# Performance work log

Measured on AMD Instinct MI355X. Metric: run time of the kernel, lower is better.

## Reference

```python
import jax, jax.numpy as jnp
import numpy as np

A_DIM = 12      # action dim (half of augmented state)
N_STEPS = 10    # Heun ODE steps (Flow.N)
P = 0.95        # mixing coefficient in _Heun_method


def _mlp(x, obs, t, W1, b1, W2, b2, W3, b3, W4, b4):
    h = jnp.concatenate([x, obs, t], axis=-1)
    h = jnp.tanh(h @ W1 + b1)
    h = jnp.tanh(h @ W2 + b2)
    h = jnp.tanh(h @ W3 + b3)
    return h @ W4 + b4


def _heun(obs, x, params):
    # Flow._Heun_method: sequential Heun integration of the augmented state.
    z = x[..., :A_DIM]
    y = x[..., A_DIM:]
    dt = 1.0 / N_STEPS
    tshape = x.shape[:-1] + (1,)

    def step(carry, i):
        z, y = carry
        t = jnp.ones(tshape, x.dtype) * (i / N_STEPS)
        z_t = _mlp(y, obs, t, *params)
        z_in = z + z_t * dt
        y_t = _mlp(z_in, obs, t, *params)
        y_in = y + y_t * dt
        z_new = P * z_in + (1.0 - P) * y_in
        y_new = P * y_in + (1.0 - P) * z_new
        return (z_new, y_new), None

    (z, y), _ = jax.lax.scan(step, (z, y), jnp.arange(N_STEPS, dtype=x.dtype))
    return jnp.concatenate([z, y], axis=-1)


def setup_inputs() -> dict:
    key = jax.random.key(0)
    ks = jax.random.split(key, 8)
    B, OBS, H, A = 2048, 48, 256, A_DIM
    din = A + OBS + 1  # 61
    s = 0.05  # small init scale to keep tanh unsaturated
    return {
        "observations": jax.random.normal(ks[0], (B, OBS), jnp.float32),
        "action_aug_0": jax.random.normal(ks[1], (B, 2 * A), jnp.float32),
        "W1": s * jax.random.normal(ks[2], (din, H), jnp.float32),
        "b1": jnp.zeros((H,), jnp.float32),
        "W2": s * jax.random.normal(ks[3], (H, H), jnp.float32),
        "b2": jnp.zeros((H,), jnp.float32),
        "W3": s * jax.random.normal(ks[4], (H, H), jnp.float32),
        "b3": jnp.zeros((H,), jnp.float32),
        "W4": s * jax.random.normal(ks[5], (H, A), jnp.float32),
        "b4": jnp.zeros((A,), jnp.float32),
        "jac": 1,
    }


def reference(observations, action_aug_0, W1, b1, W2, b2, W3, b3, W4, b4, jac):
    params = (W1, b1, W2, b2, W3, b3, W4, b4)
    action_aug = _heun(observations, action_aug_0, params)
    d = action_aug_0.shape[-1]
    # Normal(0, I) log prob summed over dims
    log_probs = -0.5 * jnp.sum(action_aug_0 ** 2, axis=-1) - 0.5 * d * jnp.log(2.0 * jnp.pi)
    if jac:
        single = lambda o, x: _heun(o, x, params)  # per-sample (obs_dim,), (2a,)
        J = jax.vmap(jax.jacrev(single, argnums=1))(observations, action_aug_0)  # (B, 2a, 2a)
        _, logabsdet = jnp.linalg.slogdet(J)  # = log|det J|
        log_probs = log_probs - logabsdet
    return action_aug, log_probs
```

## Files before the change

kernel.cpp:

```cpp
#include <hip/hip_runtime.h>
#include <hip/hip_bf16.h>


typedef unsigned short ushort_t;
typedef float f32x4 __attribute__((ext_vector_type(4)));
typedef short s16x8 __attribute__((ext_vector_type(8)));

#define NB      2048
#define OBS_D   48
#define HDIM    256
#define ADIM    12
#define XDIM    24
#define NSTEPS  10
#define DT      0.1f
#define PP      0.95f

#define W1U 0
#define W2U 16384
#define W3U 81920
#define W4U 147456
#define N_FRAG 151552
#define FRAG_BLOCKS 592
#define LP_BLOCKS 8

#define LDS_BUFA 0
#define LDS_BUFB 9216
#define LDS_AIN  18432
#define LDS_PART 21504
#define LDS_TOTAL 31744

__device__ __forceinline__ ushort_t f2bf(float f) {
  unsigned u = __builtin_bit_cast(unsigned, f);
  u += 0x7fffu + ((u >> 16) & 1u);
  return (ushort_t)(u >> 16);
}

__device__ __forceinline__ float tanh_fast(float x) {
  float e = __builtin_amdgcn_exp2f(x * 2.885390081777927f);
  return 1.f - 2.f * __builtin_amdgcn_rcpf(1.f + e);
}

__device__ __forceinline__ int ain_byte(int r, int c) {
  return r * 192 + ((c >> 5) << 6) + ((c & 15) << 2) + (((c >> 4) & 1) << 1);
}

__global__ void prep_kernel(const float* __restrict__ W1, const float* __restrict__ b1,
                            const float* __restrict__ W2, const float* __restrict__ W3,
                            const float* __restrict__ W4, const float* __restrict__ x0,
                            const int* __restrict__ jac, float* __restrict__ out,
                            ushort_t* __restrict__ ws) {
  int bid = blockIdx.x;
  int tid = threadIdx.x;
  if (bid < FRAG_BLOCKS) {
    int e = bid * 256 + tid;
    float val = 0.f;
    if (e < 16384) {
      int kt = e >> 13; int r = e & 8191;
      int nt = r >> 9, l = (r >> 3) & 63, j = r & 7;
      int k = kt * 32 + ((l >> 4) << 2) + (j >> 1) + ((j & 1) << 4);
      int col = nt * 16 + (l & 15);
      val = (k < 61) ? W1[k * 256 + col] : ((k == 61) ? b1[col] : 0.f);
    } else if (e < 81920) {
      int e2 = e - 16384;
      int kt = e2 >> 13; int r = e2 & 8191;
      int nt = r >> 9, l = (r >> 3) & 63, j = r & 7;
      int k = kt * 32 + ((l >> 4) << 2) + (j >> 1) + ((j & 1) << 4);
      int col = nt * 16 + (l & 15);
      val = W2[k * 256 + col];
    } else if (e < 147456) {
      int e2 = e - 81920;
      int kt = e2 >> 13; int r = e2 & 8191;
      int nt = r >> 9, l = (r >> 3) & 63, j = r & 7;
      int k = kt * 32 + ((l >> 4) << 2) + (j >> 1) + ((j & 1) << 4);
      int col = nt * 16 + (l & 15);
      val = W3[k * 256 + col];
    } else {
      int e2 = e - 147456;
      int kt = e2 >> 9; int r = e2 & 511;
      int l = (r >> 3) & 63, j = r & 7;
      int k = kt * 32 + ((l >> 4) << 2) + (j >> 1) + ((j & 1) << 4);
      int col = l & 15;
      val = (col < 12) ? W4[k * 12 + col] : 0.f;
    }
    ws[e] = f2bf(val);
  } else {
    int s = (bid - FRAG_BLOCKS) * 256 + tid;
    float acc = 0.f;
    #pragma unroll 4
    for (int j = 0; j < XDIM; ++j) { float v = x0[s * XDIM + j]; acc += v * v; }
    float C = (jac[0] != 0) ? -9.744134143900015f : -22.054524796912143f;
    out[NB * XDIM + s] = -0.5f * acc + C;
  }
}

__global__ __launch_bounds__(512, 2) void flow_main(
    const float* __restrict__ obs, const float* __restrict__ x0,
    const float* __restrict__ b2g, const float* __restrict__ b3g,
    const float* __restrict__ b4g, const ushort_t* __restrict__ ws,
    float* __restrict__ out) {
  __shared__ char lds[LDS_TOTAL];
  const int tid  = threadIdx.x;
  const int lane = tid & 63;
  const int wv   = tid >> 6;
  const int g    = lane >> 4;
  const int ar   = lane & 15;
  const int row0 = blockIdx.x * 16;

  const int aA = LDS_AIN + ar * 192 + g * 16;
  const int hA = ar * 576 + (((ar >> 2) & 1) << 6) + g * 16;
  const int hw = (g * 4) * 576 + ((g & 1) << 6) + wv * 64 + ar * 4;
  const int pw = LDS_PART + wv * 1280 + (g * 4) * 80 + ar * 4;
  const int rs = tid >> 4, cs = tid & 15;

  for (int p = tid; p < 768; p += 512) ((unsigned*)(lds + LDS_AIN))[p] = 0u;
  __syncthreads();

  for (int idx = tid; idx < 16 * OBS_D; idx += 512) {
    int r = idx / OBS_D, o = idx - r * OBS_D;
    *(ushort_t*)(lds + LDS_AIN + ain_byte(r, 12 + o)) = f2bf(obs[(row0 + r) * OBS_D + o]);
  }
  if (tid < 16)
    *(ushort_t*)(lds + LDS_AIN + tid * 192 + 118) = (ushort_t)0x3F80;

  float zr = 0.f, yr = 0.f, zir = 0.f;
  if (tid < 256 && cs < 12) {
    zr = x0[(row0 + rs) * XDIM + cs];
    yr = x0[(row0 + rs) * XDIM + 12 + cs];
    *(ushort_t*)(lds + LDS_AIN + rs * 192 + cs * 4) = f2bf(yr);
  }

  s16x8 w1r[2][2], w2r[8][2], w3r[8][2], w4r;
  #pragma unroll
  for (int kt = 0; kt < 2; ++kt)
    #pragma unroll
    for (int n = 0; n < 2; ++n)
      w1r[kt][n] = *(const s16x8*)(ws + W1U + (((kt * 16) + (2 * wv + n)) * 64 + lane) * 8);
  #pragma unroll
  for (int kt = 0; kt < 8; ++kt)
    #pragma unroll
    for (int n = 0; n < 2; ++n) {
      w2r[kt][n] = *(const s16x8*)(ws + W2U + (((kt * 16) + (2 * wv + n)) * 64 + lane) * 8);
      w3r[kt][n] = *(const s16x8*)(ws + W3U + (((kt * 16) + (2 * wv + n)) * 64 + lane) * 8);
    }
  w4r = *(const s16x8*)(ws + W4U + (wv * 64 + lane) * 8);

  float b2r[2], b3r[2];
  #pragma unroll
  for (int n = 0; n < 2; ++n) {
    b2r[n] = b2g[(2 * wv + n) * 16 + ar];
    b3r[n] = b3g[(2 * wv + n) * 16 + ar];
  }
  const float b4v = (cs < 12) ? b4g[cs] : 0.f;

  __syncthreads();

  const f32x4 z4 = {0.f, 0.f, 0.f, 0.f};

  for (int i = 0; i < NSTEPS; ++i) {
    #pragma unroll
    for (int ev = 0; ev < 2; ++ev) {
      f32x4 acc0 = z4, acc1 = z4;
      #pragma unroll
      for (int kt = 0; kt < 2; ++kt) {
        s16x8 a = *(const s16x8*)(lds + aA + kt * 64);
        acc0 = __builtin_amdgcn_mfma_f32_16x16x32_bf16(a, w1r[kt][0], acc0, 0, 0, 0);
        acc1 = __builtin_amdgcn_mfma_f32_16x16x32_bf16(a, w1r[kt][1], acc1, 0, 0, 0);
      }
      #pragma unroll
      for (int r = 0; r < 4; ++r) {
        unsigned p = (unsigned)f2bf(tanh_fast(acc0[r]))
                   | ((unsigned)f2bf(tanh_fast(acc1[r])) << 16);
        *(unsigned*)(lds + LDS_BUFA + hw + r * 576) = p;
      }
      __syncthreads();

      acc0 = z4; acc1 = z4;
      #pragma unroll
      for (int kt = 0; kt < 8; ++kt) {
        s16x8 a = *(const s16x8*)(lds + LDS_BUFA + hA + kt * 64);
        acc0 = __builtin_amdgcn_mfma_f32_16x16x32_bf16(a, w2r[kt][0], acc0, 0, 0, 0);
        acc1 = __builtin_amdgcn_mfma_f32_16x16x32_bf16(a, w2r[kt][1], acc1, 0, 0, 0);
      }
      #pragma unroll
      for (int r = 0; r < 4; ++r) {
        unsigned p = (unsigned)f2bf(tanh_fast(acc0[r] + b2r[0]))
                   | ((unsigned)f2bf(tanh_fast(acc1[r] + b2r[1])) << 16);
        *(unsigned*)(lds + LDS_BUFB + hw + r * 576) = p;
      }
      __syncthreads();

      acc0 = z4; acc1 = z4;
      #pragma unroll
      for (int kt = 0; kt < 8; ++kt) {
        s16x8 a = *(const s16x8*)(lds + LDS_BUFB + hA + kt * 64);
        acc0 = __builtin_amdgcn_mfma_f32_16x16x32_bf16(a, w3r[kt][0], acc0, 0, 0, 0);
        acc1 = __builtin_amdgcn_mfma_f32_16x16x32_bf16(a, w3r[kt][1], acc1, 0, 0, 0);
      }
      #pragma unroll
      for (int r = 0; r < 4; ++r) {
        unsigned p = (unsigned)f2bf(tanh_fast(acc0[r] + b3r[0]))
                   | ((unsigned)f2bf(tanh_fast(acc1[r] + b3r[1])) << 16);
        *(unsigned*)(lds + LDS_BUFA + hw + r * 576) = p;
      }

      asm volatile("s_waitcnt lgkmcnt(0)" ::: "memory");
      __builtin_amdgcn_sched_barrier(0);
      {
        s16x8 a = *(const s16x8*)(lds + LDS_BUFA + hA + wv * 64);
        f32x4 p4 = __builtin_amdgcn_mfma_f32_16x16x32_bf16(a, w4r, z4, 0, 0, 0);
        #pragma unroll
        for (int r = 0; r < 4; ++r)
          *(float*)(lds + pw + r * 80) = p4[r];
      }
      __syncthreads();

      if (tid < 256) {
        float s = b4v;
        #pragma unroll
        for (int w = 0; w < 8; ++w)
          s += *(const float*)(lds + LDS_PART + w * 1280 + rs * 80 + cs * 4);
        if (cs < 12) {
          if (ev == 0) {
            zir = zr + DT * s;
            *(ushort_t*)(lds + LDS_AIN + rs * 192 + cs * 4) = f2bf(zir);
          } else {
            float yi = yr + DT * s;
            zr = PP * zir + (1.f - PP) * yi;
            yr = PP * yi + (1.f - PP) * zr;
            *(ushort_t*)(lds + LDS_AIN + rs * 192 + cs * 4) = f2bf(yr);
          }
        }
        if (ev == 1 && cs == 15)
          *(ushort_t*)(lds + LDS_AIN + rs * 192 + 114) = f2bf((float)(i + 1) * DT);
      }
      __syncthreads();
    }
  }

  if (tid < 256 && cs < 12) {
    out[(row0 + rs) * XDIM + cs]      = zr;
    out[(row0 + rs) * XDIM + 12 + cs] = yr;
  }
}

extern "C" void kernel_launch(void* const* d_in, const int* in_sizes, int n_in,
                              void* d_out, int out_size, void* d_ws, size_t ws_size,
                              hipStream_t stream) {
  const float* obs = (const float*)d_in[0];
  const float* x0  = (const float*)d_in[1];
  const float* W1  = (const float*)d_in[2];
  const float* b1  = (const float*)d_in[3];
  const float* W2  = (const float*)d_in[4];
  const float* b2  = (const float*)d_in[5];
  const float* W3  = (const float*)d_in[6];
  const float* b3  = (const float*)d_in[7];
  const float* W4  = (const float*)d_in[8];
  const float* b4  = (const float*)d_in[9];
  const int*   jac = (const int*)d_in[10];
  float* out = (float*)d_out;
  ushort_t* ws = (ushort_t*)d_ws;

  prep_kernel<<<FRAG_BLOCKS + LP_BLOCKS, 256, 0, stream>>>(W1, b1, W2, W3, W4, x0, jac, out, ws);
  flow_main<<<128, 512, 0, stream>>>(obs, x0, b2, b3, b4, ws, out);
}
```

Measured before the change: 49.71 us.

## Halve rows per block, swizzle LDS layout, split MFMA accumulator chains

Each block now handles 8 real rows instead of 16 and the grid doubles to 256 blocks, so more CUs take part in the sequential Heun loop. The padded LDS layouts are replaced with XOR-swizzled 128/512-byte row layouts to avoid bank conflicts at lower memory cost. The 8-deep MFMA accumulation for layers 2 and 3 is split into two independent chains that are summed afterwards, shortening the dependency latency. Empty asm constraints pin the weight fragments in registers. The cost is that half of each MFMA tile now works on padding rows, and the full weight set is loaded by twice as many blocks.

Measured after the change: 50.84 us. 2.3% more time.

```diff
diff --git a/kernel.cpp b/kernel.cpp
--- a/kernel.cpp
+++ b/kernel.cpp
@@ -8,8 +8,6 @@
 
 #define NB      2048
 #define OBS_D   48
-#define HDIM    256
-#define ADIM    12
 #define XDIM    24
 #define NSTEPS  10
 #define DT      0.1f
@@ -19,15 +17,14 @@
 #define W2U 16384
 #define W3U 81920
 #define W4U 147456
-#define N_FRAG 151552
 #define FRAG_BLOCKS 592
 #define LP_BLOCKS 8
 
 #define LDS_BUFA 0
-#define LDS_BUFB 9216
-#define LDS_AIN  18432
-#define LDS_PART 21504
-#define LDS_TOTAL 31744
+#define LDS_BUFB 8192
+#define LDS_AIN  16384
+#define LDS_PART 18432
+#define LDS_TOTAL 27648
 
 __device__ __forceinline__ ushort_t f2bf(float f) {
   unsigned u = __builtin_bit_cast(unsigned, f);
@@ -41,7 +38,8 @@
 }
 
 __device__ __forceinline__ int ain_byte(int r, int c) {
-  return r * 192 + ((c >> 5) << 6) + ((c & 15) << 2) + (((c >> 4) & 1) << 1);
+  int cb = ((c >> 5) << 6) | ((c & 15) << 2) | (((c >> 4) & 1) << 1);
+  return r * 128 + (cb ^ ((r & 7) << 4));
 }
 
 __global__ void prep_kernel(const float* __restrict__ W1, const float* __restrict__ b1,
@@ -104,29 +102,26 @@
   const int wv   = tid >> 6;
   const int g    = lane >> 4;
   const int ar   = lane & 15;
-  const int row0 = blockIdx.x * 16;
-
-  const int aA = LDS_AIN + ar * 192 + g * 16;
-  const int hA = ar * 576 + (((ar >> 2) & 1) << 6) + g * 16;
-  const int hw = (g * 4) * 576 + ((g & 1) << 6) + wv * 64 + ar * 4;
-  const int pw = LDS_PART + wv * 1280 + (g * 4) * 80 + ar * 4;
-  const int rs = tid >> 4, cs = tid & 15;
-
-  for (int p = tid; p < 768; p += 512) ((unsigned*)(lds + LDS_AIN))[p] = 0u;
+  const int row0 = blockIdx.x * 8;
+  const int sw   = (ar & 7) << 4;
+  const int hwc  = wv * 64 + ar * 4;
+  const int rs   = tid >> 4, cs = tid & 15;
+
+  ((unsigned*)(lds + LDS_AIN))[tid] = 0u;
   __syncthreads();
 
-  for (int idx = tid; idx < 16 * OBS_D; idx += 512) {
-    int r = idx / OBS_D, o = idx - r * OBS_D;
+  if (tid < 8 * OBS_D) {
+    int r = tid / OBS_D, o = tid - r * OBS_D;
     *(ushort_t*)(lds + LDS_AIN + ain_byte(r, 12 + o)) = f2bf(obs[(row0 + r) * OBS_D + o]);
   }
   if (tid < 16)
-    *(ushort_t*)(lds + LDS_AIN + tid * 192 + 118) = (ushort_t)0x3F80;
+    *(ushort_t*)(lds + LDS_AIN + tid * 128 + (118 ^ ((tid & 7) << 4))) = (ushort_t)0x3F80;
 
   float zr = 0.f, yr = 0.f, zir = 0.f;
-  if (tid < 256 && cs < 12) {
+  if (tid < 256 && cs < 12 && rs < 8) {
     zr = x0[(row0 + rs) * XDIM + cs];
     yr = x0[(row0 + rs) * XDIM + 12 + cs];
-    *(ushort_t*)(lds + LDS_AIN + rs * 192 + cs * 4) = f2bf(yr);
+    *(ushort_t*)(lds + LDS_AIN + rs * 128 + ((cs * 4) ^ ((rs & 7) << 4))) = f2bf(yr);
   }
 
   s16x8 w1r[2][2], w2r[8][2], w3r[8][2], w4r;
@@ -143,6 +138,13 @@
       w3r[kt][n] = *(const s16x8*)(ws + W3U + (((kt * 16) + (2 * wv + n)) * 64 + lane) * 8);
     }
   w4r = *(const s16x8*)(ws + W4U + (wv * 64 + lane) * 8);
+  #pragma unroll
+  for (int kt = 0; kt < 2; ++kt)
+    asm volatile("" : "+v"(w1r[kt][0]), "+v"(w1r[kt][1]));
+  #pragma unroll
+  for (int kt = 0; kt < 8; ++kt)
+    asm volatile("" : "+v"(w2r[kt][0]), "+v"(w2r[kt][1]), "+v"(w3r[kt][0]), "+v"(w3r[kt][1]));
+  asm volatile("" : "+v"(w4r));
 
   float b2r[2], b3r[2];
   #pragma unroll
@@ -162,55 +164,68 @@
       f32x4 acc0 = z4, acc1 = z4;
       #pragma unroll
       for (int kt = 0; kt < 2; ++kt) {
-        s16x8 a = *(const s16x8*)(lds + aA + kt * 64);
+        s16x8 a = *(const s16x8*)(lds + LDS_AIN + ar * 128 + ((kt * 64 + g * 16) ^ sw));
         acc0 = __builtin_amdgcn_mfma_f32_16x16x32_bf16(a, w1r[kt][0], acc0, 0, 0, 0);
         acc1 = __builtin_amdgcn_mfma_f32_16x16x32_bf16(a, w1r[kt][1], acc1, 0, 0, 0);
       }
       #pragma unroll
       for (int r = 0; r < 4; ++r) {
+        int rw = g * 4 + r;
         unsigned p = (unsigned)f2bf(tanh_fast(acc0[r]))
                    | ((unsigned)f2bf(tanh_fast(acc1[r])) << 16);
-        *(unsigned*)(lds + LDS_BUFA + hw + r * 576) = p;
-      }
-      __syncthreads();
-
-      acc0 = z4; acc1 = z4;
-      #pragma unroll
-      for (int kt = 0; kt < 8; ++kt) {
-        s16x8 a = *(const s16x8*)(lds + LDS_BUFA + hA + kt * 64);
-        acc0 = __builtin_amdgcn_mfma_f32_16x16x32_bf16(a, w2r[kt][0], acc0, 0, 0, 0);
-        acc1 = __builtin_amdgcn_mfma_f32_16x16x32_bf16(a, w2r[kt][1], acc1, 0, 0, 0);
-      }
+        *(unsigned*)(lds + LDS_BUFA + rw * 512 + (hwc ^ ((rw & 7) << 4))) = p;
+      }
+      __syncthreads();
+
+      f32x4 a0a = z4, a0b = z4, a1a = z4, a1b = z4;
+      #pragma unroll
+      for (int kt = 0; kt < 4; ++kt) {
+        s16x8 a = *(const s16x8*)(lds + LDS_BUFA + ar * 512 + ((kt * 64 + g * 16) ^ sw));
+        s16x8 b = *(const s16x8*)(lds + LDS_BUFA + ar * 512 + (((kt + 4) * 64 + g * 16) ^ sw));
+        a0a = __builtin_amdgcn_mfma_f32_16x16x32_bf16(a, w2r[kt][0], a0a, 0, 0, 0);
+        a1a = __builtin_amdgcn_mfma_f32_16x16x32_bf16(a, w2r[kt][1], a1a, 0, 0, 0);
+        a0b = __builtin_amdgcn_mfma_f32_16x16x32_bf16(b, w2r[kt + 4][0], a0b, 0, 0, 0);
+        a1b = __builtin_amdgcn_mfma_f32_16x16x32_bf16(b, w2r[kt + 4][1], a1b, 0, 0, 0);
+      }
+      acc0 = a0a + a0b; acc1 = a1a + a1b;
       #pragma unroll
       for (int r = 0; r < 4; ++r) {
+        int rw = g * 4 + r;
         unsigned p = (unsigned)f2bf(tanh_fast(acc0[r] + b2r[0]))
                    | ((unsigned)f2bf(tanh_fast(acc1[r] + b2r[1])) << 16);
-        *(unsigned*)(lds + LDS_BUFB + hw + r * 576) = p;
-      }
-      __syncthreads();
-
-      acc0 = z4; acc1 = z4;
-      #pragma unroll
-      for (int kt = 0; kt < 8; ++kt) {
-        s16x8 a = *(const s16x8*)(lds + LDS_BUFB + hA + kt * 64);
-        acc0 = __builtin_amdgcn_mfma_f32_16x16x32_bf16(a, w3r[kt][0], acc0, 0, 0, 0);
-        acc1 = __builtin_amdgcn_mfma_f32_16x16x32_bf16(a, w3r[kt][1], acc1, 0, 0, 0);
-      }
+        *(unsigned*)(lds + LDS_BUFB + rw * 512 + (hwc ^ ((rw & 7) << 4))) = p;
+      }
+      __syncthreads();
+
+      a0a = z4; a0b = z4; a1a = z4; a1b = z4;
+      #pragma unroll
+      for (int kt = 0; kt < 4; ++kt) {
+        s16x8 a = *(const s16x8*)(lds + LDS_BUFB + ar * 512 + ((kt * 64 + g * 16) ^ sw));
+        s16x8 b = *(const s16x8*)(lds + LDS_BUFB + ar * 512 + (((kt + 4) * 64 + g * 16) ^ sw));
+        a0a = __builtin_amdgcn_mfma_f32_16x16x32_bf16(a, w3r[kt][0], a0a, 0, 0, 0);
+        a1a = __builtin_amdgcn_mfma_f32_16x16x32_bf16(a, w3r[kt][1], a1a, 0, 0, 0);
+        a0b = __builtin_amdgcn_mfma_f32_16x16x32_bf16(b, w3r[kt + 4][0], a0b, 0, 0, 0);
+        a1b = __builtin_amdgcn_mfma_f32_16x16x32_bf16(b, w3r[kt + 4][1], a1b, 0, 0, 0);
+      }
+      acc0 = a0a + a0b; acc1 = a1a + a1b;
       #pragma unroll
       for (int r = 0; r < 4; ++r) {
+        int rw = g * 4 + r;
         unsigned p = (unsigned)f2bf(tanh_fast(acc0[r] + b3r[0]))
                    | ((unsigned)f2bf(tanh_fast(acc1[r] + b3r[1])) << 16);
-        *(unsigned*)(lds + LDS_BUFA + hw + r * 576) = p;
+        *(unsigned*)(lds + LDS_BUFA + rw * 512 + (hwc ^ ((rw & 7) << 4))) = p;
       }
 
       asm volatile("s_waitcnt lgkmcnt(0)" ::: "memory");
       __builtin_amdgcn_sched_barrier(0);
       {
-        s16x8 a = *(const s16x8*)(lds + LDS_BUFA + hA + wv * 64);
+        s16x8 a = *(const s16x8*)(lds + LDS_BUFA + ar * 512 + ((wv * 64 + g * 16) ^ sw));
         f32x4 p4 = __builtin_amdgcn_mfma_f32_16x16x32_bf16(a, w4r, z4, 0, 0, 0);
         #pragma unroll
-        for (int r = 0; r < 4; ++r)
-          *(float*)(lds + pw + r * 80) = p4[r];
+        for (int r = 0; r < 4; ++r) {
+          int rw = g * 4 + r;
+          *(float*)(lds + LDS_PART + wv * 1152 + rw * 72 + ar * 4) = p4[r];
+        }
       }
       __syncthreads();
 
@@ -218,26 +233,28 @@
         float s = b4v;
         #pragma unroll
         for (int w = 0; w < 8; ++w)
-          s += *(const float*)(lds + LDS_PART + w * 1280 + rs * 80 + cs * 4);
+          s += *(const float*)(lds + LDS_PART + w * 1152 + rs * 72 + cs * 4);
         if (cs < 12) {
+          int byt = rs * 128 + ((cs * 4) ^ ((rs & 7) << 4));
           if (ev == 0) {
             zir = zr + DT * s;
-            *(ushort_t*)(lds + LDS_AIN + rs * 192 + cs * 4) = f2bf(zir);
+            *(ushort_t*)(lds + LDS_AIN + byt) = f2bf(zir);
           } else {
             float yi = yr + DT * s;
             zr = PP * zir + (1.f - PP) * yi;
             yr = PP * yi + (1.f - PP) * zr;
-            *(ushort_t*)(lds + LDS_AIN + rs * 192 + cs * 4) = f2bf(yr);
+            *(ushort_t*)(lds + LDS_AIN + byt) = f2bf(yr);
           }
         }
         if (ev == 1 && cs == 15)
-          *(ushort_t*)(lds + LDS_AIN + rs * 192 + 114) = f2bf((float)(i + 1) * DT);
+          *(ushort_t*)(lds + LDS_AIN + rs * 128 + (114 ^ ((rs & 7) << 4))) =
+              f2bf((float)(i + 1) * DT);
       }
       __syncthreads();
     }
   }
 
-  if (tid < 256 && cs < 12) {
+  if (tid < 256 && cs < 12 && rs < 8) {
     out[(row0 + rs) * XDIM + cs]      = zr;
     out[(row0 + rs) * XDIM + 12 + cs] = yr;
   }
@@ -261,5 +278,5 @@
   ushort_t* ws = (ushort_t*)d_ws;
 
   prep_kernel<<<FRAG_BLOCKS + LP_BLOCKS, 256, 0, stream>>>(W1, b1, W2, W3, W4, x0, jac, out, ws);
-  flow_main<<<128, 512, 0, stream>>>(obs, x0, b2, b3, b4, ws, out);
-}
+  flow_main<<<256, 512, 0, stream>>>(obs, x0, b2, b3, b4, ws, out);
+}
```
